# Kernel tuning notes

Measured on AMD Instinct MI355X. Metric: run time of the kernel, lower is better.

The kernel has to match this reference:

```python
import jax, jax.numpy as jnp
import numpy as np
from jax import lax

# Key identity used: modulating ALL weights of output channel o by s_o (with no bias
# inside the modulated conv, as in the source where F.conv2d(..., bias=None)) is
# mathematically identical to a plain conv followed by per-(batch, out_channel)
# scaling of the output. This collapses the per-sample Python loop into one conv.

def _upsample2x(x):
    # nearest-neighbor x2, matching F.interpolate(scale_factor=2) default mode
    return jnp.repeat(jnp.repeat(x, 2, axis=2), 2, axis=3)

def _conv(x, w):
    return lax.conv_general_dilated(
        x, w, window_strides=(1, 1), padding=[(1, 1), (1, 1)],
        dimension_numbers=("NCHW", "OIHW", "NCHW"))

def _modconv(x, style, w, fc_w, fc_b):
    # style_fc: [B, style_dim] -> [B, out_ch]
    s = style @ fc_w.T + fc_b          # [B, O]
    y = _conv(x, w)                    # [B, O, H, W]
    return y * s[:, :, None, None]


def setup_inputs() -> dict:
    key = jax.random.key(0)
    ks = jax.random.split(key, 16)
    B, SD = 8, 512
    chans = [(512, 256), (256, 128), (128, 64), (64, 64), (64, 64)]
    inp = {
        "x": jax.random.normal(ks[0], (B, 512, 8, 8), jnp.float32),
        "style": jax.random.normal(ks[1], (B, SD), jnp.float32),
    }
    for i, (ci, co) in enumerate(chans, start=1):
        inp[f"w{i}"] = jax.random.normal(ks[2 * i], (co, ci, 3, 3), jnp.float32) * (1.0 / np.sqrt(ci * 9))
        inp[f"fw{i}"] = jax.random.normal(ks[2 * i + 1], (co, SD), jnp.float32) * (1.0 / np.sqrt(SD))
        inp[f"fb{i}"] = jnp.ones((co,), jnp.float32)
    inp["wf"] = jax.random.normal(ks[12], (3, 64, 3, 3), jnp.float32) * (1.0 / np.sqrt(64 * 9))
    inp["bf"] = jnp.zeros((3,), jnp.float32)
    return inp


def reference(x, style, w1, fw1, fb1, w2, fw2, fb2, w3, fw3, fb3,
              w4, fw4, fb4, w5, fw5, fb5, wf, bf):
    x = _upsample2x(x)
    x = jax.nn.relu(_modconv(x, style, w1, fw1, fb1))
    x = _upsample2x(x)
    x = jax.nn.relu(_modconv(x, style, w2, fw2, fb2))
    x = _upsample2x(x)
    x = jax.nn.relu(_modconv(x, style, w3, fw3, fb3))
    x = _upsample2x(x)
    x = jax.nn.relu(_modconv(x, style, w4, fw4, fb4))
    x = _upsample2x(x)
    x = jax.nn.relu(_modconv(x, style, w5, fw5, fb5))
    x = _conv(x, wf) + bf[None, :, None, None]
    return x
```

## Files before the change

### kernel.cpp

```cpp
#include <hip/hip_runtime.h>
#include <hip/hip_bf16.h>
#include <cstddef>

typedef __bf16 bf16x8 __attribute__((ext_vector_type(8)));
typedef float f32x4 __attribute__((ext_vector_type(4)));


__global__ void convert_x_kernel(const float* __restrict__ x, __hip_bfloat16* __restrict__ act0) {
    int t = blockIdx.x * 256 + threadIdx.x;
    int c = t & 511; int rest = t >> 9;
    int w = rest & 7; rest >>= 3; int h = rest & 7; int b = rest >> 3;
    act0[t] = __float2bfloat16(x[((b * 512 + c) * 8 + h) * 8 + w]);
}

__global__ void wtrans_all_kernel(const float* __restrict__ w1, __hip_bfloat16* __restrict__ o1,
                                  const float* __restrict__ w2, __hip_bfloat16* __restrict__ o2,
                                  const float* __restrict__ w3, __hip_bfloat16* __restrict__ o3,
                                  const float* __restrict__ w4, __hip_bfloat16* __restrict__ o4,
                                  const float* __restrict__ w5, __hip_bfloat16* __restrict__ o5,
                                  const float* __restrict__ wf, __hip_bfloat16* __restrict__ of) {
    int t = blockIdx.x * 256 + threadIdx.x;
    if (t >= 1688576) return;
    if (t < 1548288) {
        const float* w; __hip_bfloat16* o; int lgci, lgco;
        if      (t < 1179648) { w = w1; o = o1; lgci = 9; lgco = 8; }
        else if (t < 1474560) { t -= 1179648; w = w2; o = o2; lgci = 8; lgco = 7; }
        else                  { t -= 1474560; w = w3; o = o3; lgci = 7; lgco = 6; }
        int CI = 1 << lgci;
        int ci = t & (CI - 1);
        int co = (t >> lgci) & ((1 << lgco) - 1);
        int tap = t >> (lgci + lgco);
        o[t] = __float2bfloat16(w[((size_t)co * CI + ci) * 9 + tap]);
    } else if (t < 1679360) {
        int u = t - 1548288;
        const float* w; __hip_bfloat16* o;
        if (u < 65536) { w = w4; o = o4; }
        else           { u -= 65536; w = w5; o = o5; }
        int j   = u & 7;
        int ln  = (u >> 3) & 63;
        int ch  = (u >> 9) & 1;
        int nt  = (u >> 10) & 3;
        int tp  = (u >> 12) & 3;
        int cls = (u >> 14) & 3;
        int py = cls >> 1, px = cls & 1;
        int i = tp >> 1, jj = tp & 1;
        int co = nt * 16 + (ln & 15);
        int ci = ch * 32 + (ln >> 4) * 8 + j;
        int r0 = i * (1 + py), rc = py ? (2 - i) : (1 + i);
        int c0 = jj * (1 + px), cc = px ? (2 - jj) : (1 + jj);
        const float* wb = w + ((size_t)co * 64 + ci) * 9;
        float s = 0.f;
        for (int rr = 0; rr < rc; ++rr)
            for (int c2 = 0; c2 < cc; ++c2)
                s += wb[(r0 + rr) * 3 + (c0 + c2)];
        o[u] = __float2bfloat16(s);
    } else {
        int u = t - 1679360;
        int j  = u & 7;
        int ln = (u >> 3) & 63;
        int ch = (u >> 9) & 1;
        int tap = u >> 10;
        int rr = ln & 15, qq = ln >> 4;
        int ci = ch * 32 + qq * 8 + j;
        float v = (rr < 3) ? wf[((size_t)rr * 64 + ci) * 9 + tap] : 0.f;
        of[u] = __float2bfloat16(v);
    }
}

__global__ void style_all_kernel(const float* __restrict__ style,
                                 const float* __restrict__ fw1, const float* __restrict__ fb1,
                                 const float* __restrict__ fw2, const float* __restrict__ fb2,
                                 const float* __restrict__ fw3, const float* __restrict__ fb3,
                                 const float* __restrict__ fw4, const float* __restrict__ fb4,
                                 const float* __restrict__ fw5, const float* __restrict__ fb5,
                                 float* __restrict__ S) {
    int wvid = blockIdx.x * 4 + (threadIdx.x >> 6);
    int lane = threadIdx.x & 63;
    const float* fw; const float* fb; int lg, sOff, local;
    if      (wvid < 2048) { fw = fw1; fb = fb1; lg = 8; sOff = 0;    local = wvid; }
    else if (wvid < 3072) { fw = fw2; fb = fb2; lg = 7; sOff = 2048; local = wvid - 2048; }
    else if (wvid < 3584) { fw = fw3; fb = fb3; lg = 6; sOff = 3072; local = wvid - 3072; }
    else if (wvid < 4096) { fw = fw4; fb = fb4; lg = 6; sOff = 3584; local = wvid - 3584; }
    else                  { fw = fw5; fb = fb5; lg = 6; sOff = 4096; local = wvid - 4096; }
    int b = local >> lg, o = local & ((1 << lg) - 1);
    const float* sb = style + b * 512;
    const float* fwo = fw + (size_t)o * 512;
    float p = 0.f;
    #pragma unroll
    for (int k = lane; k < 512; k += 64) p += sb[k] * fwo[k];
    #pragma unroll
    for (int off = 32; off > 0; off >>= 1) p += __shfl_down(p, off);
    if (lane == 0) S[sOff + local] = p + fb[o];
}

template <int CI, int CO, int HS, int WS>
__launch_bounds__(512)
__global__ void conv_partial_kernel(const __hip_bfloat16* __restrict__ actIn,
                                    const __hip_bfloat16* __restrict__ wtr,
                                    float* __restrict__ Part) {
    constexpr int HO = HS * 2, WO = WS * 2;
    constexpr size_t sliceN = (size_t)8 * HO * WO * CO;
    const int tid = threadIdx.x;
    const int lane = tid & 63, wv = tid >> 6;
    const int r = lane & 15, q = lane >> 4;
    const int pw = WO / 16, ppb = (HO / 16) * pw;
    const int b = blockIdx.x / ppb;
    const int prest = blockIdx.x - b * ppb;
    const int ph = prest / pw, pwi = prest - ph * pw;
    const int oh0 = ph * 16, ow0 = pwi * 16;
    const int sh0 = oh0 >> 1, sw0 = ow0 >> 1;
    const int n0 = blockIdx.y * 64;
    const int ciOff = blockIdx.z * 64;

    __shared__ alignas(16) __hip_bfloat16 Tile[100 * 72];
    __shared__ alignas(16) __hip_bfloat16 Wlds[2][64 * 72];

    f32x4 acc[2][4];
    #pragma unroll
    for (int i = 0; i < 2; ++i)
        #pragma unroll
        for (int j = 0; j < 4; ++j) acc[i][j] = f32x4{0.f, 0.f, 0.f, 0.f};

    for (int i = tid; i < 800; i += 512) {
        int pix = i >> 3, koct = i & 7;
        int tr = pix / 10, tc2 = pix - tr * 10;
        int su = sh0 - 1 + tr, sv = sw0 - 1 + tc2;
        uint4 v = {0, 0, 0, 0};
        if (su >= 0 && su < HS && sv >= 0 && sv < WS)
            v = *(const uint4*)(actIn + ((size_t)((b * HS + su) * WS + sv) * CI + ciOff + koct * 8));
        *(uint4*)&Tile[pix * 72 + koct * 8] = v;
    }
    {
        int co = tid >> 3, koct = tid & 7;
        *(uint4*)&Wlds[0][co * 72 + koct * 8] =
            *(const uint4*)(wtr + ((size_t)(n0 + co)) * CI + ciOff + koct * 8);
    }
    __syncthreads();

    #pragma unroll 1
    for (int tap = 0; tap < 9; ++tap) {
        const bool pf = (tap < 8);
        uint4 wr0 = {0,0,0,0};
        if (pf) {
            int co0 = tid >> 3, k0 = tid & 7;
            wr0 = *(const uint4*)(wtr + ((size_t)(tap + 1) * CO + n0 + co0) * CI + ciOff + k0 * 8);
        }
        const int dyv = tap / 3;
        const int dxm1 = tap - dyv * 3 - 1;
        const int tc = ((r + dxm1) >> 1) + 1;
        int apix[2];
        #pragma unroll
        for (int mt = 0; mt < 2; ++mt)
            apix[mt] = ((((wv * 2 + mt) + dyv - 1) >> 1) + 1) * 10 + tc;

        const int buf = tap & 1;
        #pragma unroll
        for (int ch = 0; ch < 2; ++ch) {
            bf16x8 af[2], bfr[4];
            #pragma unroll
            for (int mt = 0; mt < 2; ++mt)
                af[mt] = *(const bf16x8*)&Tile[apix[mt] * 72 + ch * 32 + q * 8];
            #pragma unroll
            for (int nt = 0; nt < 4; ++nt)
                bfr[nt] = *(const bf16x8*)&Wlds[buf][(nt * 16 + r) * 72 + ch * 32 + q * 8];
            #pragma unroll
            for (int mt = 0; mt < 2; ++mt)
                #pragma unroll
                for (int nt = 0; nt < 4; ++nt)
                    acc[mt][nt] = __builtin_amdgcn_mfma_f32_16x16x32_bf16(
                        af[mt], bfr[nt], acc[mt][nt], 0, 0, 0);
        }
        if (pf) {
            int nb = buf ^ 1;
            int co0 = tid >> 3, k0 = tid & 7;
            *(uint4*)&Wlds[nb][co0 * 72 + k0 * 8] = wr0;
            __syncthreads();
        }
    }

    float* P = Part + (size_t)blockIdx.z * sliceN;
    #pragma unroll
    for (int mt = 0; mt < 2; ++mt) {
        const int prow = wv * 2 + mt;
        #pragma unroll
        for (int t2 = 0; t2 < 4; ++t2) {
            const int pcol = q * 4 + t2;
            const size_t obase = ((size_t)(b * HO + oh0 + prow) * WO + ow0 + pcol) * CO + n0;
            #pragma unroll
            for (int nt = 0; nt < 4; ++nt)
                P[obase + nt * 16 + r] = acc[mt][nt][t2];
        }
    }
}

template <int KS, int CO, int HW>
__launch_bounds__(256)
__global__ void reduce_kernel(const float* __restrict__ Part, const float* __restrict__ S,
                              __hip_bfloat16* __restrict__ actOut) {
    constexpr size_t sliceN = (size_t)8 * HW * CO;
    size_t e = ((size_t)blockIdx.x * 256 + threadIdx.x) * 4;
    if (e >= sliceN) return;
    f32x4 sum = {0.f, 0.f, 0.f, 0.f};
    #pragma unroll
    for (int k = 0; k < KS; ++k) sum += *(const f32x4*)(Part + (size_t)k * sliceN + e);
    const int co = (int)(e & (CO - 1));
    const int b = (int)(e / ((size_t)HW * CO));
    const float* Sb = S + b * CO + co;
    union { ushort4 u; __hip_bfloat16 h[4]; } pack;
    #pragma unroll
    for (int j = 0; j < 4; ++j)
        pack.h[j] = __float2bfloat16(fmaxf(sum[j] * Sb[j], 0.f));
    *(ushort4*)((unsigned short*)actOut + e) = pack.u;
}

template <int HS, int WS>
__launch_bounds__(256)
__global__ void conv_patch_kernel(const __hip_bfloat16* __restrict__ actIn,
                                  const __hip_bfloat16* __restrict__ wpk,
                                  const float* __restrict__ S,
                                  __hip_bfloat16* __restrict__ actOut) {
    constexpr int HO = HS * 2, WO = WS * 2;

    const int tid = threadIdx.x;
    const int lane = tid & 63, wv = tid >> 6;
    const int r = lane & 15, q = lane >> 4;
    const int rs = r >> 3, sc = r & 7;
    const int lane8 = lane * 8;
    const int py = wv >> 1, px = wv & 1;

    const int pw = WO / 16, ppb = (HO / 16) * pw;
    const int b = blockIdx.x / ppb;
    const int prest = blockIdx.x - b * ppb;
    const int ph = prest / pw, pwi = prest - ph * pw;
    const int oh0 = ph * 16, ow0 = pwi * 16;
    const int sh0 = oh0 >> 1, sw0 = ow0 >> 1;

    __shared__ alignas(16) __hip_bfloat16 Tile[100 * 72];

    f32x4 acc[4][4];
    #pragma unroll
    for (int i = 0; i < 4; ++i)
        #pragma unroll
        for (int j = 0; j < 4; ++j) acc[i][j] = f32x4{0.f, 0.f, 0.f, 0.f};

    for (int i = tid; i < 800; i += 256) {
        int pix = i >> 3, koct = i & 7;
        int tr = pix / 10, tc2 = pix - tr * 10;
        int su = sh0 - 1 + tr, sv = sw0 - 1 + tc2;
        uint4 v = {0, 0, 0, 0};
        if (su >= 0 && su < HS && sv >= 0 && sv < WS)
            v = *(const uint4*)(actIn + ((size_t)((b * HS + su) * WS + sv) * 64 + koct * 8));
        *(uint4*)&Tile[pix * 72 + koct * 8] = v;
    }
    __syncthreads();

    const __hip_bfloat16* wcls = wpk + ((size_t)wv << 14);

    bf16x8 bA[4][2], bB[4][2];

    auto loadB = [&](bf16x8 (&dst)[4][2], int tp) {
        #pragma unroll
        for (int nt = 0; nt < 4; ++nt)
            #pragma unroll
            for (int ch = 0; ch < 2; ++ch)
                dst[nt][ch] = *(const bf16x8*)(wcls + (tp << 12) + ((nt * 2 + ch) << 9) + lane8);
    };

    auto compute = [&](int tp, bf16x8 (&bfr)[4][2]) {
        const int i = tp >> 1, j = tp & 1;
        const int ro = i + py, co2 = j + px;
        int apix[4];
        #pragma unroll
        for (int mt = 0; mt < 4; ++mt)
            apix[mt] = (2 * mt + rs + ro) * 10 + (sc + co2);
        #pragma unroll
        for (int ch = 0; ch < 2; ++ch) {
            bf16x8 af[4];
            #pragma unroll
            for (int mt = 0; mt < 4; ++mt)
                af[mt] = *(const bf16x8*)&Tile[apix[mt] * 72 + ch * 32 + q * 8];
            #pragma unroll
            for (int mt = 0; mt < 4; ++mt)
                #pragma unroll
                for (int nt = 0; nt < 4; ++nt)
                    acc[mt][nt] = __builtin_amdgcn_mfma_f32_16x16x32_bf16(
                        af[mt], bfr[nt][ch], acc[mt][nt], 0, 0, 0);
        }
    };

    loadB(bA, 0);
    loadB(bB, 1);
    compute(0, bA);
    loadB(bA, 2);
    compute(1, bB);
    loadB(bB, 3);
    compute(2, bA);
    compute(3, bB);

    float sv_[4];
    #pragma unroll
    for (int nt = 0; nt < 4; ++nt) sv_[nt] = S[b * 64 + nt * 16 + r];
    #pragma unroll
    for (int mt = 0; mt < 4; ++mt) {
        #pragma unroll
        for (int t2 = 0; t2 < 4; ++t2) {
            const int m = q * 4 + t2;
            const int row = oh0 + 4 * mt + 2 * (m >> 3) + py;
            const int col = ow0 + 2 * (m & 7) + px;
            const size_t obase = ((size_t)(b * HO + row) * WO + col) * 64;
            #pragma unroll
            for (int nt = 0; nt < 4; ++nt)
                actOut[obase + nt * 16 + r] =
                    __float2bfloat16(fmaxf(acc[mt][nt][t2] * sv_[nt], 0.f));
        }
    }
}

__launch_bounds__(256)
__global__ void conv_final_kernel(const __hip_bfloat16* __restrict__ actIn,
                                  const __hip_bfloat16* __restrict__ wpkF,
                                  const float* __restrict__ bias,
                                  float* __restrict__ out) {
    constexpr int HO = 256, WO = 256;
    const int tid = threadIdx.x, lane = tid & 63, wv = tid >> 6;
    const int r = lane & 15, q = lane >> 4;
    const int lane8 = lane * 8;

    const int ppb = 32 * 16;
    const int b = blockIdx.x / ppb;
    const int prest = blockIdx.x - b * ppb;
    const int ph = prest >> 4, pwi = prest & 15;
    const int oh0 = ph * 8, ow0 = pwi * 16;

    __shared__ alignas(16) __hip_bfloat16 Tile[10 * 18 * 72];

    for (int i = tid; i < 1440; i += 256) {
        int pix = i >> 3, koct = i & 7;
        int tr = pix / 18, tc2 = pix - tr * 18;
        int u = oh0 - 1 + tr, v = ow0 - 1 + tc2;
        uint4 val = {0, 0, 0, 0};
        if (u >= 0 && u < HO && v >= 0 && v < WO)
            val = *(const uint4*)(actIn + ((size_t)((b * HO + u) * WO + v) * 64 + koct * 8));
        *(uint4*)&Tile[pix * 72 + koct * 8] = val;
    }
    __syncthreads();

    f32x4 acc[2];
    acc[0] = f32x4{0.f, 0.f, 0.f, 0.f};
    acc[1] = f32x4{0.f, 0.f, 0.f, 0.f};

    #pragma unroll 1
    for (int tap = 0; tap < 9; ++tap) {
        const int dyv = tap / 3;
        const int dxv = tap - dyv * 3;
        const int tc = r + dxv;
        int apix[2];
        #pragma unroll
        for (int mt = 0; mt < 2; ++mt)
            apix[mt] = (wv * 2 + mt + dyv) * 18 + tc;
        #pragma unroll
        for (int ch = 0; ch < 2; ++ch) {
            bf16x8 bfr = *(const bf16x8*)(wpkF + ((tap * 2 + ch) << 9) + lane8);
            #pragma unroll
            for (int mt = 0; mt < 2; ++mt) {
                bf16x8 af = *(const bf16x8*)&Tile[apix[mt] * 72 + ch * 32 + q * 8];
                acc[mt] = __builtin_amdgcn_mfma_f32_16x16x32_bf16(af, bfr, acc[mt], 0, 0, 0);
            }
        }
    }

    if (r < 3) {
        const float bs = bias[r];
        #pragma unroll
        for (int mt = 0; mt < 2; ++mt) {
            const int prow = wv * 2 + mt;
            #pragma unroll
            for (int t2 = 0; t2 < 4; ++t2) {
                const int pcol = q * 4 + t2;
                out[((size_t)(b * 3 + r) << 16) + (oh0 + prow) * 256 + ow0 + pcol] =
                    acc[mt][t2] + bs;
            }
        }
    }
}

extern "C" void kernel_launch(void* const* d_in, const int* in_sizes, int n_in,
                              void* d_out, int out_size, void* d_ws, size_t ws_size,
                              hipStream_t stream) {
    const float* x    = (const float*)d_in[0];
    const float* sty  = (const float*)d_in[1];
    const float* w1   = (const float*)d_in[2];
    const float* fw1  = (const float*)d_in[3];
    const float* fb1  = (const float*)d_in[4];
    const float* w2   = (const float*)d_in[5];
    const float* fw2  = (const float*)d_in[6];
    const float* fb2  = (const float*)d_in[7];
    const float* w3   = (const float*)d_in[8];
    const float* fw3  = (const float*)d_in[9];
    const float* fb3  = (const float*)d_in[10];
    const float* w4   = (const float*)d_in[11];
    const float* fw4  = (const float*)d_in[12];
    const float* fb4  = (const float*)d_in[13];
    const float* w5   = (const float*)d_in[14];
    const float* fw5  = (const float*)d_in[15];
    const float* fb5  = (const float*)d_in[16];
    const float* wf   = (const float*)d_in[17];
    const float* bf   = (const float*)d_in[18];
    float* out = (float*)d_out;

    char* ws = (char*)d_ws;
    size_t off = 0;
    auto alloc = [&](size_t bytes) {
        char* p = ws + off;
        off += (bytes + 255) & ~(size_t)255;
        return p;
    };
    float* S1 = (float*)alloc(8 * 256 * 4);
    float* S2 = (float*)alloc(8 * 128 * 4);
    float* S3 = (float*)alloc(8 * 64 * 4);
    float* S4 = (float*)alloc(8 * 64 * 4);
    float* S5 = (float*)alloc(8 * 64 * 4);
    __hip_bfloat16* act0 = (__hip_bfloat16*)alloc((size_t)262144 * 2);
    __hip_bfloat16* act1 = (__hip_bfloat16*)alloc((size_t)524288 * 2);
    __hip_bfloat16* act2 = (__hip_bfloat16*)alloc((size_t)1048576 * 2);
    __hip_bfloat16* act3 = (__hip_bfloat16*)alloc((size_t)2097152 * 2);
    __hip_bfloat16* act4 = (__hip_bfloat16*)alloc((size_t)8388608 * 2);
    __hip_bfloat16* act5 = (__hip_bfloat16*)alloc((size_t)33554432 * 2);
    __hip_bfloat16* wt1  = (__hip_bfloat16*)alloc((size_t)9 * 256 * 512 * 2);
    __hip_bfloat16* wt2  = (__hip_bfloat16*)alloc((size_t)9 * 128 * 256 * 2);
    __hip_bfloat16* wt3  = (__hip_bfloat16*)alloc((size_t)9 * 64 * 128 * 2);
    __hip_bfloat16* wt4  = (__hip_bfloat16*)alloc((size_t)65536 * 2);
    __hip_bfloat16* wt5  = (__hip_bfloat16*)alloc((size_t)65536 * 2);
    __hip_bfloat16* wtF  = (__hip_bfloat16*)alloc((size_t)9 * 16 * 64 * 2);
    if (off > ws_size) return;

    float* Part = (float*)act5;

    convert_x_kernel<<<1024, 256, 0, stream>>>(x, act0);
    wtrans_all_kernel<<<6596, 256, 0, stream>>>(w1, wt1, w2, wt2, w3, wt3,
                                                w4, wt4, w5, wt5, wf, wtF);
    style_all_kernel<<<1152, 256, 0, stream>>>(sty, fw1, fb1, fw2, fb2, fw3, fb3,
                                               fw4, fb4, fw5, fb5, S1);

    conv_partial_kernel<512, 256, 8, 8><<<dim3(8, 4, 8), 512, 0, stream>>>(act0, wt1, Part);
    reduce_kernel<8, 256, 256><<<512, 256, 0, stream>>>(Part, S1, act1);
    conv_partial_kernel<256, 128, 16, 16><<<dim3(32, 2, 4), 512, 0, stream>>>(act1, wt2, Part);
    reduce_kernel<4, 128, 1024><<<1024, 256, 0, stream>>>(Part, S2, act2);
    conv_partial_kernel<128, 64, 32, 32><<<dim3(128, 1, 2), 512, 0, stream>>>(act2, wt3, Part);
    reduce_kernel<2, 64, 4096><<<2048, 256, 0, stream>>>(Part, S3, act3);

    conv_patch_kernel<64, 64><<<dim3(512), 256, 0, stream>>>(act3, wt4, S4, act4);
    conv_patch_kernel<128, 128><<<dim3(2048), 256, 0, stream>>>(act4, wt5, S5, act5);
    conv_final_kernel<<<4096, 256, 0, stream>>>(act5, wtF, bf, out);
}
```

Measured before the change: 217.4 us.

## Merge prep kernels into one launch and read final conv input directly

```diff
diff --git a/kernel.cpp b/kernel.cpp
--- a/kernel.cpp
+++ b/kernel.cpp
@@ -5,92 +5,92 @@
 typedef __bf16 bf16x8 __attribute__((ext_vector_type(8)));
 typedef float f32x4 __attribute__((ext_vector_type(4)));
 
-
-__global__ void convert_x_kernel(const float* __restrict__ x, __hip_bfloat16* __restrict__ act0) {
-    int t = blockIdx.x * 256 + threadIdx.x;
-    int c = t & 511; int rest = t >> 9;
-    int w = rest & 7; rest >>= 3; int h = rest & 7; int b = rest >> 3;
-    act0[t] = __float2bfloat16(x[((b * 512 + c) * 8 + h) * 8 + w]);
-}
-
-__global__ void wtrans_all_kernel(const float* __restrict__ w1, __hip_bfloat16* __restrict__ o1,
-                                  const float* __restrict__ w2, __hip_bfloat16* __restrict__ o2,
-                                  const float* __restrict__ w3, __hip_bfloat16* __restrict__ o3,
-                                  const float* __restrict__ w4, __hip_bfloat16* __restrict__ o4,
-                                  const float* __restrict__ w5, __hip_bfloat16* __restrict__ o5,
-                                  const float* __restrict__ wf, __hip_bfloat16* __restrict__ of) {
-    int t = blockIdx.x * 256 + threadIdx.x;
-    if (t >= 1688576) return;
-    if (t < 1548288) {
-        const float* w; __hip_bfloat16* o; int lgci, lgco;
-        if      (t < 1179648) { w = w1; o = o1; lgci = 9; lgco = 8; }
-        else if (t < 1474560) { t -= 1179648; w = w2; o = o2; lgci = 8; lgco = 7; }
-        else                  { t -= 1474560; w = w3; o = o3; lgci = 7; lgco = 6; }
-        int CI = 1 << lgci;
-        int ci = t & (CI - 1);
-        int co = (t >> lgci) & ((1 << lgco) - 1);
-        int tap = t >> (lgci + lgco);
-        o[t] = __float2bfloat16(w[((size_t)co * CI + ci) * 9 + tap]);
-    } else if (t < 1679360) {
-        int u = t - 1548288;
-        const float* w; __hip_bfloat16* o;
-        if (u < 65536) { w = w4; o = o4; }
-        else           { u -= 65536; w = w5; o = o5; }
-        int j   = u & 7;
-        int ln  = (u >> 3) & 63;
-        int ch  = (u >> 9) & 1;
-        int nt  = (u >> 10) & 3;
-        int tp  = (u >> 12) & 3;
-        int cls = (u >> 14) & 3;
-        int py = cls >> 1, px = cls & 1;
-        int i = tp >> 1, jj = tp & 1;
-        int co = nt * 16 + (ln & 15);
-        int ci = ch * 32 + (ln >> 4) * 8 + j;
-        int r0 = i * (1 + py), rc = py ? (2 - i) : (1 + i);
-        int c0 = jj * (1 + px), cc = px ? (2 - jj) : (1 + jj);
-        const float* wb = w + ((size_t)co * 64 + ci) * 9;
-        float s = 0.f;
-        for (int rr = 0; rr < rc; ++rr)
-            for (int c2 = 0; c2 < cc; ++c2)
-                s += wb[(r0 + rr) * 3 + (c0 + c2)];
-        o[u] = __float2bfloat16(s);
+__global__ void prep_all_kernel(const float* __restrict__ x, __hip_bfloat16* __restrict__ act0,
+                                const float* __restrict__ w1, __hip_bfloat16* __restrict__ o1,
+                                const float* __restrict__ w2, __hip_bfloat16* __restrict__ o2,
+                                const float* __restrict__ w3, __hip_bfloat16* __restrict__ o3,
+                                const float* __restrict__ w4, __hip_bfloat16* __restrict__ o4,
+                                const float* __restrict__ w5, __hip_bfloat16* __restrict__ o5,
+                                const float* __restrict__ wf, __hip_bfloat16* __restrict__ of,
+                                const float* __restrict__ style,
+                                const float* __restrict__ fw1, const float* __restrict__ fb1,
+                                const float* __restrict__ fw2, const float* __restrict__ fb2,
+                                const float* __restrict__ fw3, const float* __restrict__ fb3,
+                                const float* __restrict__ fw4, const float* __restrict__ fb4,
+                                const float* __restrict__ fw5, const float* __restrict__ fb5,
+                                float* __restrict__ S) {
+    const int blk = blockIdx.x;
+    if (blk < 1024) {
+        int t = blk * 256 + threadIdx.x;
+        int c = t & 511; int rest = t >> 9;
+        int w = rest & 7; rest >>= 3; int h = rest & 7; int b = rest >> 3;
+        act0[t] = __float2bfloat16(x[((b * 512 + c) * 8 + h) * 8 + w]);
+    } else if (blk < 7620) {
+        int t = (blk - 1024) * 256 + threadIdx.x;
+        if (t >= 1688576) return;
+        if (t < 1548288) {
+            const float* w; __hip_bfloat16* o; int lgci, lgco;
+            if      (t < 1179648) { w = w1; o = o1; lgci = 9; lgco = 8; }
+            else if (t < 1474560) { t -= 1179648; w = w2; o = o2; lgci = 8; lgco = 7; }
+            else                  { t -= 1474560; w = w3; o = o3; lgci = 7; lgco = 6; }
+            int CI = 1 << lgci;
+            int ci = t & (CI - 1);
+            int co = (t >> lgci) & ((1 << lgco) - 1);
+            int tap = t >> (lgci + lgco);
+            o[t] = __float2bfloat16(w[((size_t)co * CI + ci) * 9 + tap]);
+        } else if (t < 1679360) {
+            int u = t - 1548288;
+            const float* w; __hip_bfloat16* o;
+            if (u < 65536) { w = w4; o = o4; }
+            else           { u -= 65536; w = w5; o = o5; }
+            int j   = u & 7;
+            int ln  = (u >> 3) & 63;
+            int ch  = (u >> 9) & 1;
+            int nt  = (u >> 10) & 3;
+            int tp  = (u >> 12) & 3;
+            int cls = (u >> 14) & 3;
+            int py = cls >> 1, px = cls & 1;
+            int i = tp >> 1, jj = tp & 1;
+            int co = nt * 16 + (ln & 15);
+            int ci = ch * 32 + (ln >> 4) * 8 + j;
+            int r0 = i * (1 + py), rc = py ? (2 - i) : (1 + i);
+            int c0 = jj * (1 + px), cc = px ? (2 - jj) : (1 + jj);
+            const float* wb = w + ((size_t)co * 64 + ci) * 9;
+            float s = 0.f;
+            for (int rr = 0; rr < rc; ++rr)
+                for (int c2 = 0; c2 < cc; ++c2)
+                    s += wb[(r0 + rr) * 3 + (c0 + c2)];
+            o[u] = __float2bfloat16(s);
+        } else {
+            int u = t - 1679360;
+            int j  = u & 7;
+            int ln = (u >> 3) & 63;
+            int ch = (u >> 9) & 1;
+            int tap = u >> 10;
+            int rr = ln & 15, qq = ln >> 4;
+            int ci = ch * 32 + qq * 8 + j;
+            float v = (rr < 3) ? wf[((size_t)rr * 64 + ci) * 9 + tap] : 0.f;
+            of[u] = __float2bfloat16(v);
+        }
     } else {
-        int u = t - 1679360;
-        int j  = u & 7;
-        int ln = (u >> 3) & 63;
-        int ch = (u >> 9) & 1;
-        int tap = u >> 10;
-        int rr = ln & 15, qq = ln >> 4;
-        int ci = ch * 32 + qq * 8 + j;
-        float v = (rr < 3) ? wf[((size_t)rr * 64 + ci) * 9 + tap] : 0.f;
-        of[u] = __float2bfloat16(v);
-    }
-}
-
-__global__ void style_all_kernel(const float* __restrict__ style,
-                                 const float* __restrict__ fw1, const float* __restrict__ fb1,
-                                 const float* __restrict__ fw2, const float* __restrict__ fb2,
-                                 const float* __restrict__ fw3, const float* __restrict__ fb3,
-                                 const float* __restrict__ fw4, const float* __restrict__ fb4,
-                                 const float* __restrict__ fw5, const float* __restrict__ fb5,
-                                 float* __restrict__ S) {
-    int wvid = blockIdx.x * 4 + (threadIdx.x >> 6);
-    int lane = threadIdx.x & 63;
-    const float* fw; const float* fb; int lg, sOff, local;
-    if      (wvid < 2048) { fw = fw1; fb = fb1; lg = 8; sOff = 0;    local = wvid; }
-    else if (wvid < 3072) { fw = fw2; fb = fb2; lg = 7; sOff = 2048; local = wvid - 2048; }
-    else if (wvid < 3584) { fw = fw3; fb = fb3; lg = 6; sOff = 3072; local = wvid - 3072; }
-    else if (wvid < 4096) { fw = fw4; fb = fb4; lg = 6; sOff = 3584; local = wvid - 3584; }
-    else                  { fw = fw5; fb = fb5; lg = 6; sOff = 4096; local = wvid - 4096; }
-    int b = local >> lg, o = local & ((1 << lg) - 1);
-    const float* sb = style + b * 512;
-    const float* fwo = fw + (size_t)o * 512;
-    float p = 0.f;
-    #pragma unroll
-    for (int k = lane; k < 512; k += 64) p += sb[k] * fwo[k];
-    #pragma unroll
-    for (int off = 32; off > 0; off >>= 1) p += __shfl_down(p, off);
-    if (lane == 0) S[sOff + local] = p + fb[o];
+        int wvid = (blk - 7620) * 4 + (threadIdx.x >> 6);
+        int lane = threadIdx.x & 63;
+        const float* fw; const float* fb; int lg, sOff, local;
+        if      (wvid < 2048) { fw = fw1; fb = fb1; lg = 8; sOff = 0;    local = wvid; }
+        else if (wvid < 3072) { fw = fw2; fb = fb2; lg = 7; sOff = 2048; local = wvid - 2048; }
+        else if (wvid < 3584) { fw = fw3; fb = fb3; lg = 6; sOff = 3072; local = wvid - 3072; }
+        else if (wvid < 4096) { fw = fw4; fb = fb4; lg = 6; sOff = 3584; local = wvid - 3584; }
+        else                  { fw = fw5; fb = fb5; lg = 6; sOff = 4096; local = wvid - 4096; }
+        int b = local >> lg, o = local & ((1 << lg) - 1);
+        const float* sb = style + b * 512;
+        const float* fwo = fw + (size_t)o * 512;
+        float p = 0.f;
+        #pragma unroll
+        for (int k = lane; k < 512; k += 64) p += sb[k] * fwo[k];
+        #pragma unroll
+        for (int off = 32; off > 0; off >>= 1) p += __shfl_down(p, off);
+        if (lane == 0) S[sOff + local] = p + fb[o];
+    }
 }
 
 template <int CI, int CO, int HS, int WS>
@@ -321,49 +321,38 @@
                                   const __hip_bfloat16* __restrict__ wpkF,
                                   const float* __restrict__ bias,
                                   float* __restrict__ out) {
-    constexpr int HO = 256, WO = 256;
     const int tid = threadIdx.x, lane = tid & 63, wv = tid >> 6;
     const int r = lane & 15, q = lane >> 4;
     const int lane8 = lane * 8;
 
-    const int ppb = 32 * 16;
-    const int b = blockIdx.x / ppb;
-    const int prest = blockIdx.x - b * ppb;
-    const int ph = prest >> 4, pwi = prest & 15;
-    const int oh0 = ph * 8, ow0 = pwi * 16;
-
-    __shared__ alignas(16) __hip_bfloat16 Tile[10 * 18 * 72];
-
-    for (int i = tid; i < 1440; i += 256) {
-        int pix = i >> 3, koct = i & 7;
-        int tr = pix / 18, tc2 = pix - tr * 18;
-        int u = oh0 - 1 + tr, v = ow0 - 1 + tc2;
-        uint4 val = {0, 0, 0, 0};
-        if (u >= 0 && u < HO && v >= 0 && v < WO)
-            val = *(const uint4*)(actIn + ((size_t)((b * HO + u) * WO + v) * 64 + koct * 8));
-        *(uint4*)&Tile[pix * 72 + koct * 8] = val;
-    }
-    __syncthreads();
-
-    f32x4 acc[2];
-    acc[0] = f32x4{0.f, 0.f, 0.f, 0.f};
-    acc[1] = f32x4{0.f, 0.f, 0.f, 0.f};
+    int bid = blockIdx.x;
+    const int cseg = bid & 3;  bid >>= 2;
+    const int rgrp = bid & 63; bid >>= 6;
+    const int b = bid;
+    const int orow = rgrp * 4 + wv;
+    const int col0 = cseg * 64;
+
+    f32x4 acc[4];
+    #pragma unroll
+    for (int i = 0; i < 4; ++i) acc[i] = f32x4{0.f, 0.f, 0.f, 0.f};
+
+    const __hip_bfloat16* actB = actIn + ((size_t)b << 22);
 
     #pragma unroll 1
     for (int tap = 0; tap < 9; ++tap) {
-        const int dyv = tap / 3;
-        const int dxv = tap - dyv * 3;
-        const int tc = r + dxv;
-        int apix[2];
-        #pragma unroll
-        for (int mt = 0; mt < 2; ++mt)
-            apix[mt] = (wv * 2 + mt + dyv) * 18 + tc;
+        const int dy = tap / 3, dx = tap - 3 * dy;
+        const int srow = orow + dy - 1;
+        if (srow < 0 || srow > 255) continue;
+        const __hip_bfloat16* rowp = actB + ((size_t)srow << 14);
         #pragma unroll
         for (int ch = 0; ch < 2; ++ch) {
             bf16x8 bfr = *(const bf16x8*)(wpkF + ((tap * 2 + ch) << 9) + lane8);
             #pragma unroll
-            for (int mt = 0; mt < 2; ++mt) {
-                bf16x8 af = *(const bf16x8*)&Tile[apix[mt] * 72 + ch * 32 + q * 8];
+            for (int mt = 0; mt < 4; ++mt) {
+                const int scol = col0 + mt * 16 + r + dx - 1;
+                bf16x8 af = bf16x8{0, 0, 0, 0, 0, 0, 0, 0};
+                if (scol >= 0 && scol < 256)
+                    af = *(const bf16x8*)(rowp + (scol << 6) + ch * 32 + q * 8);
                 acc[mt] = __builtin_amdgcn_mfma_f32_16x16x32_bf16(af, bfr, acc[mt], 0, 0, 0);
             }
         }
@@ -372,15 +361,11 @@
     if (r < 3) {
         const float bs = bias[r];
         #pragma unroll
-        for (int mt = 0; mt < 2; ++mt) {
-            const int prow = wv * 2 + mt;
-            #pragma unroll
-            for (int t2 = 0; t2 < 4; ++t2) {
-                const int pcol = q * 4 + t2;
-                out[((size_t)(b * 3 + r) << 16) + (oh0 + prow) * 256 + ow0 + pcol] =
+        for (int mt = 0; mt < 4; ++mt)
+            #pragma unroll
+            for (int t2 = 0; t2 < 4; ++t2)
+                out[((size_t)(b * 3 + r) << 16) + orow * 256 + col0 + mt * 16 + q * 4 + t2] =
                     acc[mt][t2] + bs;
-            }
-        }
     }
 }
 
@@ -436,11 +421,11 @@
 
     float* Part = (float*)act5;
 
-    convert_x_kernel<<<1024, 256, 0, stream>>>(x, act0);
-    wtrans_all_kernel<<<6596, 256, 0, stream>>>(w1, wt1, w2, wt2, w3, wt3,
-                                                w4, wt4, w5, wt5, wf, wtF);
-    style_all_kernel<<<1152, 256, 0, stream>>>(sty, fw1, fb1, fw2, fb2, fw3, fb3,
-                                               fw4, fb4, fw5, fb5, S1);
+    prep_all_kernel<<<8772, 256, 0, stream>>>(x, act0,
+                                              w1, wt1, w2, wt2, w3, wt3,
+                                              w4, wt4, w5, wt5, wf, wtF,
+                                              sty, fw1, fb1, fw2, fb2, fw3, fb3,
+                                              fw4, fb4, fw5, fb5, S1);
 
     conv_partial_kernel<512, 256, 8, 8><<<dim3(8, 4, 8), 512, 0, stream>>>(act0, wt1, Part);
     reduce_kernel<8, 256, 256><<<512, 256, 0, stream>>>(Part, S1, act1);
@@ -451,5 +436,6 @@
 
     conv_patch_kernel<64, 64><<<dim3(512), 256, 0, stream>>>(act3, wt4, S4, act4);
     conv_patch_kernel<128, 128><<<dim3(2048), 256, 0, stream>>>(act4, wt5, S5, act5);
-    conv_final_kernel<<<4096, 256, 0, stream>>>(act5, wtF, bf, out);
-}
+
+    conv_final_kernel<<<2048, 256, 0, stream>>>(act5, wtF, bf, out);
+}
```

New measurement: 349.2 us. +60.6%, slower.
